# Kernel optimization log

Hardware: AMD Instinct MI355X
Metric: run time of the kernel (lower is better)

Reference implementation:

```python
import jax, jax.numpy as jnp
import numpy as np

BOUNDS = 1.3
RES = 512
N_COMP = 16
N_LAMB = 3        # n_lamb_params[0]
VEC_PARAM = 3     # vecSize_params[0]
OUT_DIM = 32
N_PTS = 2097152

MAT_X = np.array([0, 0, 1])  # matMode first coord per plane
MAT_Y = np.array([1, 2, 2])  # matMode second coord per plane
VEC_M = np.array([2, 1, 0])  # vecMode


def _sample2d(grid, x, y):
    # grid: [C,H,W]; x,y: [N] in [-1,1]; bilinear, align_corners=True
    C, H, W = grid.shape
    ix = (x + 1.0) * 0.5 * (W - 1)
    iy = (y + 1.0) * 0.5 * (H - 1)
    x0 = jnp.floor(ix)
    y0 = jnp.floor(iy)
    wx = ix - x0
    wy = iy - y0
    x0i = jnp.clip(x0.astype(jnp.int32), 0, W - 1)
    x1i = jnp.clip(x0i + 1, 0, W - 1)
    y0i = jnp.clip(y0.astype(jnp.int32), 0, H - 1)
    y1i = jnp.clip(y0i + 1, 0, H - 1)
    g = lambda yi, xi: grid[:, yi, xi]  # [C,N]
    return (g(y0i, x0i) * (1 - wy) * (1 - wx) + g(y0i, x1i) * (1 - wy) * wx
            + g(y1i, x0i) * wy * (1 - wx) + g(y1i, x1i) * wy * wx)


def _sample1d(vec, y):
    # vec: [C,L]; y: [N] in [-1,1]; linear interp along L (grid width is 1,
    # x coord is always 0 in the torch code so it reduces to 1D)
    C, L = vec.shape
    iy = (y + 1.0) * 0.5 * (L - 1)
    y0 = jnp.floor(iy)
    wy = iy - y0
    y0i = jnp.clip(y0.astype(jnp.int32), 0, L - 1)
    y1i = jnpp_clip = jnp.clip(y0i + 1, 0, L - 1)
    return vec[:, y0i] * (1 - wy) + vec[:, y1i] * wy


def setup_inputs() -> dict:
    key = jax.random.key(0)
    k1, k2, k3, k4, k5 = jax.random.split(key, 5)
    pts = (jax.random.uniform(k1, (N_PTS, 3), jnp.float32) * 2.0 - 1.0) * BOUNDS
    timestamps = jax.random.uniform(k2, (N_PTS, 1), jnp.float32) * 2.0 - 1.0
    scale = 0.1
    planes = scale * jax.random.normal(k3, (3, N_COMP, RES, RES), jnp.float32)
    lines = scale * jax.random.normal(k4, (3, N_COMP, RES), jnp.float32)
    params_grid = scale * jnp.ones((N_LAMB, VEC_PARAM), jnp.float32)
    # torch Linear(19 -> 32, bias=False): weight [out, in]
    W = jax.random.normal(k5, (OUT_DIM, N_COMP + N_LAMB), jnp.float32) * (1.0 / np.sqrt(N_COMP + N_LAMB))
    return {"pts": pts, "timestamps": timestamps, "planes": planes,
            "lines": lines, "params_grid": params_grid, "W": W}


def reference(pts, timestamps, planes, lines, params_grid, W):
    # normalize_aabb with aabb = [[b,b,b],[-b,-b,-b]]
    pts_n = (pts - BOUNDS) * (2.0 / (-2.0 * BOUNDS)) - 1.0  # -> [-1,1]
    # torch code detaches sampling coordinates
    pts_n = jax.lax.stop_gradient(pts_n)
    t = jax.lax.stop_gradient(timestamps[:, 0])
    plane_x = pts_n[:, MAT_X].T  # [3,N]
    plane_y = pts_n[:, MAT_Y].T  # [3,N]
    line_c = pts_n[:, VEC_M].T   # [3,N]
    plane_feat = jax.vmap(_sample2d)(planes, plane_x, plane_y)  # [3,C,N]
    line_feat = jax.vmap(_sample1d)(lines, line_c)              # [3,C,N]
    coef = jnp.sum(plane_feat * line_feat, axis=0)              # [C,N]
    pfeat = _sample1d(params_grid, t)                           # [3,N]
    feats = jnp.concatenate([coef, pfeat], axis=0).T            # [N,19]
    return feats @ W.T                                          # [N,32]
```

## Files before the change

### kernel.cpp

```cpp
#include <hip/hip_runtime.h>
#include <hip/hip_bf16.h>

#define RES 512
#define NC 16
#define NPLANES 3
#define NB 32
#define NCELLS (NB * NB * NB)

typedef float f32x4 __attribute__((ext_vector_type(4)));

static __device__ inline float nt_loadf(const float* p) { return __builtin_nontemporal_load(p); }
static __device__ inline void nt_store4(float* p, f32x4 v) {
  __builtin_nontemporal_store(v, (f32x4*)p);
}
static __device__ inline float bf_lo(unsigned u) { return __uint_as_float(u << 16); }
static __device__ inline float bf_hi(unsigned u) { return __uint_as_float(u & 0xFFFF0000u); }

#define NORM_K ((float)(2.0 / (-2.0 * 1.3)))

__global__ __launch_bounds__(256) void transpose_planes_k(
    const float* __restrict__ in, __hip_bfloat16* __restrict__ out)
{
  __shared__ float sm[NC][64 + 1];
  int b   = blockIdx.x;
  int xb  = b & 7;
  int y   = (b >> 3) & 511;
  int p   = b >> 12;
  int x0  = xb << 6;
  int tid = threadIdx.x;
#pragma unroll
  for (int k = 0; k < 4; ++k) {
    int e = tid + k * 256;
    int c = e >> 6, x = e & 63;
    sm[c][x] = nt_loadf(&in[(size_t)((p * NC + c) * RES + y) * RES + x0 + x]);
  }
  __syncthreads();
#pragma unroll
  for (int k = 0; k < 4; ++k) {
    int e = tid + k * 256;
    int x = e >> 4, c = e & 15;
    out[(size_t)((p * RES + y) * RES + x0 + x) * NC + c] = __float2bfloat16(sm[c][x]);
  }
}

__global__ void transpose_lines_k(const float* __restrict__ in, float* __restrict__ out)
{
  int i = blockIdx.x * 256 + threadIdx.x;
  if (i >= NPLANES * RES * NC) return;
  int c = i & 15;
  int l = (i >> 4) & 511;
  int p = i >> 13;
  out[i] = nt_loadf(&in[(p * NC + c) * RES + l]);
}

static __device__ inline int cell_of(float px, float py, float pz)
{
  float n0 = (px - 1.3f) * NORM_K - 1.0f;
  float n1 = (py - 1.3f) * NORM_K - 1.0f;
  float n2 = (pz - 1.3f) * NORM_K - 1.0f;
  int cx = (int)((n0 + 1.0f) * 16.0f); cx = cx < 0 ? 0 : (cx > NB - 1 ? NB - 1 : cx);
  int cy = (int)((n1 + 1.0f) * 16.0f); cy = cy < 0 ? 0 : (cy > NB - 1 ? NB - 1 : cy);
  int cz = (int)((n2 + 1.0f) * 16.0f); cz = cz < 0 ? 0 : (cz > NB - 1 ? NB - 1 : cz);
  return (cx << 10) | (cy << 5) | cz;
}

__global__ void zero_hist_k(unsigned* __restrict__ hist)
{
  int i = blockIdx.x * 256 + threadIdx.x;
  if (i < NCELLS) hist[i] = 0;
}

__global__ __launch_bounds__(256) void histrank_k(
    const float* __restrict__ pts, unsigned* __restrict__ hist,
    unsigned* __restrict__ key, unsigned* __restrict__ rank, int N)
{
  int base = (blockIdx.x * 256 + threadIdx.x) * 4;
  if (base >= N) return;
  uint4 kv, rv;
  if (base + 4 <= N) {
    const f32x4* p4 = (const f32x4*)(pts + 3 * (size_t)base);
    f32x4 a = p4[0], b = p4[1], c = p4[2];
    int c0 = cell_of(a.x, a.y, a.z);
    int c1 = cell_of(a.w, b.x, b.y);
    int c2 = cell_of(b.z, b.w, c.x);
    int c3 = cell_of(c.y, c.z, c.w);
    kv.x = c0; kv.y = c1; kv.z = c2; kv.w = c3;
    rv.x = atomicAdd(&hist[c0], 1u);
    rv.y = atomicAdd(&hist[c1], 1u);
    rv.z = atomicAdd(&hist[c2], 1u);
    rv.w = atomicAdd(&hist[c3], 1u);
    *(uint4*)(key + base)  = kv;
    *(uint4*)(rank + base) = rv;
  } else {
    for (int j = 0; j < 4 && base + j < N; ++j) {
      int i = base + j;
      int cc = cell_of(pts[3 * i], pts[3 * i + 1], pts[3 * i + 2]);
      key[i]  = cc;
      rank[i] = atomicAdd(&hist[cc], 1u);
    }
  }
}

__global__ __launch_bounds__(256) void prefix_k(
    const unsigned* __restrict__ hist, unsigned* __restrict__ offs)
{
  __shared__ unsigned s[256];
  int t = threadIdx.x;
  unsigned sum = 0;
  for (int k = 0; k < NCELLS / 256; ++k) sum += hist[t * (NCELLS / 256) + k];
  s[t] = sum;
  __syncthreads();
  for (int d = 1; d < 256; d <<= 1) {
    unsigned v = (t >= d) ? s[t - d] : 0u;
    __syncthreads();
    s[t] += v;
    __syncthreads();
  }
  unsigned run = (t == 0) ? 0u : s[t - 1];
  for (int k = 0; k < NCELLS / 256; ++k) {
    int c = t * (NCELLS / 256) + k;
    offs[c] = run;
    run += hist[c];
  }
}

__global__ __launch_bounds__(256) void scatter_k(
    const float* __restrict__ pts, const float* __restrict__ ts,
    const unsigned* __restrict__ key, const unsigned* __restrict__ rank,
    const unsigned* __restrict__ offs, f32x4* __restrict__ rec,
    unsigned* __restrict__ oidx, int N)
{
  int base = (blockIdx.x * 256 + threadIdx.x) * 4;
  if (base >= N) return;
  if (base + 4 <= N) {
    uint4 kv = *(const uint4*)(key + base);
    uint4 rv = *(const uint4*)(rank + base);
    const f32x4* p4 = (const f32x4*)(pts + 3 * (size_t)base);
    f32x4 a = p4[0], b = p4[1], c = p4[2];
    f32x4 tv = *(const f32x4*)(ts + base);
    unsigned p0 = offs[kv.x] + rv.x;
    unsigned p1 = offs[kv.y] + rv.y;
    unsigned p2 = offs[kv.z] + rv.z;
    unsigned p3 = offs[kv.w] + rv.w;
    f32x4 r0; r0.x = a.x; r0.y = a.y; r0.z = a.z; r0.w = tv.x;
    f32x4 r1; r1.x = a.w; r1.y = b.x; r1.z = b.y; r1.w = tv.y;
    f32x4 r2; r2.x = b.z; r2.y = b.w; r2.z = c.x; r2.w = tv.z;
    f32x4 r3; r3.x = c.y; r3.y = c.z; r3.z = c.w; r3.w = tv.w;
    rec[p0] = r0; rec[p1] = r1; rec[p2] = r2; rec[p3] = r3;
    oidx[p0] = base + 0; oidx[p1] = base + 1;
    oidx[p2] = base + 2; oidx[p3] = base + 3;
  } else {
    for (int j = 0; j < 4 && base + j < N; ++j) {
      int i = base + j;
      unsigned pos = offs[key[i]] + rank[i];
      f32x4 r; r.x = pts[3 * i]; r.y = pts[3 * i + 1]; r.z = pts[3 * i + 2];
      r.w = ts[i];
      rec[pos] = r;
      oidx[pos] = i;
    }
  }
}

__global__ __launch_bounds__(256) void visnerf_sorted_k(
    const f32x4* __restrict__ rec, const unsigned* __restrict__ oidx,
    const __hip_bfloat16* __restrict__ planesb, const float* __restrict__ lines,
    const float* __restrict__ pg, const float* __restrict__ W,
    float* __restrict__ out, int N)
{
  __shared__ __align__(16) float sW[32 * 20];
  __shared__ __align__(16) float st[256 * 16];
  __shared__ float spg[9];
  int tid = threadIdx.x;
  for (int e = tid; e < 640; e += 256) {
    int o = e / 20, c = e - o * 20;
    sW[e] = (c < 19) ? W[o * 19 + c] : 0.0f;
  }
  if (tid < 9) spg[tid] = pg[tid];
  __syncthreads();

  int nwg = gridDim.x, bid = blockIdx.x;
  int sbid = ((nwg & 7) == 0) ? ((bid & 7) * (nwg >> 3) + (bid >> 3)) : bid;
  int j  = sbid * 256 + tid;
  int jc = (j < N) ? j : (N - 1);

  f32x4 r = rec[jc];
  unsigned oi = oidx[jc];
  float t = r.w;

  float nn[3];
  nn[0] = (r.x - 1.3f) * NORM_K - 1.0f;
  nn[1] = (r.y - 1.3f) * NORM_K - 1.0f;
  nn[2] = (r.z - 1.3f) * NORM_K - 1.0f;

  float feats[20];
#pragma unroll
  for (int c = 0; c < 20; ++c) feats[c] = 0.0f;

  const int matx[3] = {0, 0, 1};
  const int maty[3] = {1, 2, 2};
  const int vecm[3] = {2, 1, 0};

#pragma unroll
  for (int q = 0; q < 3; ++q) {
    float x  = nn[matx[q]], y = nn[maty[q]], lc = nn[vecm[q]];
    float ix = (x + 1.0f) * 0.5f * (float)(RES - 1);
    float iy = (y + 1.0f) * 0.5f * (float)(RES - 1);
    float fx = floorf(ix), fy = floorf(iy);
    float wx = ix - fx, wy = iy - fy;
    int x0 = (int)fx; x0 = x0 < 0 ? 0 : (x0 > RES - 1 ? RES - 1 : x0);
    int y0 = (int)fy; y0 = y0 < 0 ? 0 : (y0 > RES - 1 ? RES - 1 : y0);
    int x1 = (x0 + 1 > RES - 1) ? RES - 1 : x0 + 1;
    int y1 = (y0 + 1 > RES - 1) ? RES - 1 : y0 + 1;

    float il = (lc + 1.0f) * 0.5f * (float)(RES - 1);
    float fl = floorf(il);
    float wl = il - fl;
    int l0 = (int)fl; l0 = l0 < 0 ? 0 : (l0 > RES - 1 ? RES - 1 : l0);
    int l1 = (l0 + 1 > RES - 1) ? RES - 1 : l0 + 1;

    float w00 = (1.0f - wy) * (1.0f - wx);
    float w01 = (1.0f - wy) * wx;
    float w10 = wy * (1.0f - wx);
    float w11 = wy * wx;
    float wl0 = 1.0f - wl;

    const uint4* ta = (const uint4*)(planesb + (size_t)((q * RES + y0) * RES + x0) * NC);
    const uint4* tb = (const uint4*)(planesb + (size_t)((q * RES + y0) * RES + x1) * NC);
    const uint4* tc = (const uint4*)(planesb + (size_t)((q * RES + y1) * RES + x0) * NC);
    const uint4* td = (const uint4*)(planesb + (size_t)((q * RES + y1) * RES + x1) * NC);
    const float4* L0 = (const float4*)(lines + (size_t)(q * RES + l0) * NC);
    const float4* L1 = (const float4*)(lines + (size_t)(q * RES + l1) * NC);
#pragma unroll
    for (int h = 0; h < 2; ++h) {
      uint4 ua = ta[h], ub = tb[h], uc = tc[h], ud = td[h];
      float4 e0a = L0[2 * h + 0], e0b = L0[2 * h + 1];
      float4 e1a = L1[2 * h + 0], e1b = L1[2 * h + 1];
      const unsigned* pa = &ua.x;
      const unsigned* pb = &ub.x;
      const unsigned* pc = &uc.x;
      const unsigned* pd = &ud.x;
      const float* q0 = &e0a.x;
      const float* q1 = &e1a.x;
#pragma unroll
      for (int w = 0; w < 4; ++w) {
        int c0 = h * 8 + 2 * w;
        float pf0 = w00 * bf_lo(pa[w]) + w01 * bf_lo(pb[w]) +
                    w10 * bf_lo(pc[w]) + w11 * bf_lo(pd[w]);
        float pf1 = w00 * bf_hi(pa[w]) + w01 * bf_hi(pb[w]) +
                    w10 * bf_hi(pc[w]) + w11 * bf_hi(pd[w]);
        float lf0 = (w < 2) ? (wl0 * q0[2 * w] + wl * q1[2 * w])
                            : (wl0 * (&e0b.x)[2 * w - 4] + wl * (&e1b.x)[2 * w - 4]);
        float lf1 = (w < 2) ? (wl0 * q0[2 * w + 1] + wl * q1[2 * w + 1])
                            : (wl0 * (&e0b.x)[2 * w - 3] + wl * (&e1b.x)[2 * w - 3]);
        feats[c0 + 0] += pf0 * lf0;
        feats[c0 + 1] += pf1 * lf1;
      }
    }
  }

  {
    float it = (t + 1.0f) * 0.5f * 2.0f;
    float ft = floorf(it);
    float wt = it - ft;
    int t0 = (int)ft; t0 = t0 < 0 ? 0 : (t0 > 2 ? 2 : t0);
    int t1 = (t0 + 1 > 2) ? 2 : t0 + 1;
    feats[16] = spg[0 + t0] * (1.0f - wt) + spg[0 + t1] * wt;
    feats[17] = spg[3 + t0] * (1.0f - wt) + spg[3 + t1] * wt;
    feats[18] = spg[6 + t0] * (1.0f - wt) + spg[6 + t1] * wt;
    feats[19] = 0.0f;
  }

  int lane  = tid & 63;
  int wbase = tid & ~63;
  int chunk = lane & 3;
  int psel  = lane >> 2;
#pragma unroll
  for (int ph = 0; ph < 2; ++ph) {
#pragma unroll
    for (int o = 0; o < 16; ++o) {
      int oo = ph * 16 + o;
      const float4* wr = (const float4*)(sW + oo * 20);
      float acc = 0.0f;
#pragma unroll
      for (int k = 0; k < 5; ++k) {
        float4 wv = wr[k];
        acc += feats[4 * k + 0] * wv.x + feats[4 * k + 1] * wv.y +
               feats[4 * k + 2] * wv.z + feats[4 * k + 3] * wv.w;
      }
      st[tid * 16 + ((o + (tid >> 1)) & 15)] = acc;
    }
#pragma unroll
    for (int g = 0; g < 4; ++g) {
      int owner_lane = g * 16 + psel;
      int pt = wbase + owner_lane;
      int jp = sbid * 256 + pt;
      unsigned oi_p = (unsigned)__shfl((int)oi, owner_lane, 64);
      f32x4 v;
#pragma unroll
      for (int jj = 0; jj < 4; ++jj) {
        int o = chunk * 4 + jj;
        v[jj] = st[pt * 16 + ((o + (pt >> 1)) & 15)];
      }
      if (jp < N) nt_store4(out + (size_t)oi_p * 32 + ph * 16 + chunk * 4, v);
    }
  }
}

template <bool TP>
__global__ __launch_bounds__(256) void visnerf_main_k(
    const float* __restrict__ pts, const float* __restrict__ ts,
    const __hip_bfloat16* __restrict__ planesb, const float* __restrict__ lines,
    const float* __restrict__ planes_f32, const float* __restrict__ lines_f32,
    const float* __restrict__ pg, const float* __restrict__ W,
    float* __restrict__ out, int N)
{
  __shared__ __align__(16) float sW[32 * 20];
  __shared__ __align__(16) float st[256 * 32];
  __shared__ float spg[9];
  int tid = threadIdx.x;
  for (int e = tid; e < 640; e += 256) {
    int o = e / 20, c = e - o * 20;
    sW[e] = (c < 19) ? W[o * 19 + c] : 0.0f;
  }
  if (tid < 9) spg[tid] = pg[tid];
  __syncthreads();

  int i  = blockIdx.x * 256 + tid;
  int ii = (i < N) ? i : (N - 1);
  float px = nt_loadf(&pts[ii * 3 + 0]);
  float py = nt_loadf(&pts[ii * 3 + 1]);
  float pz = nt_loadf(&pts[ii * 3 + 2]);
  float t  = nt_loadf(&ts[ii]);

  float nn[3];
  nn[0] = (px - 1.3f) * NORM_K - 1.0f;
  nn[1] = (py - 1.3f) * NORM_K - 1.0f;
  nn[2] = (pz - 1.3f) * NORM_K - 1.0f;

  float feats[20];
#pragma unroll
  for (int c = 0; c < 20; ++c) feats[c] = 0.0f;

  const int matx[3] = {0, 0, 1};
  const int maty[3] = {1, 2, 2};
  const int vecm[3] = {2, 1, 0};

#pragma unroll
  for (int q = 0; q < 3; ++q) {
    float x  = nn[matx[q]], y = nn[maty[q]], lc = nn[vecm[q]];
    float ix = (x + 1.0f) * 0.5f * (float)(RES - 1);
    float iy = (y + 1.0f) * 0.5f * (float)(RES - 1);
    float fx = floorf(ix), fy = floorf(iy);
    float wx = ix - fx, wy = iy - fy;
    int x0 = (int)fx; x0 = x0 < 0 ? 0 : (x0 > RES - 1 ? RES - 1 : x0);
    int y0 = (int)fy; y0 = y0 < 0 ? 0 : (y0 > RES - 1 ? RES - 1 : y0);
    int x1 = (x0 + 1 > RES - 1) ? RES - 1 : x0 + 1;
    int y1 = (y0 + 1 > RES - 1) ? RES - 1 : y0 + 1;

    float il = (lc + 1.0f) * 0.5f * (float)(RES - 1);
    float fl = floorf(il);
    float wl = il - fl;
    int l0 = (int)fl; l0 = l0 < 0 ? 0 : (l0 > RES - 1 ? RES - 1 : l0);
    int l1 = (l0 + 1 > RES - 1) ? RES - 1 : l0 + 1;

    float w00 = (1.0f - wy) * (1.0f - wx);
    float w01 = (1.0f - wy) * wx;
    float w10 = wy * (1.0f - wx);
    float w11 = wy * wx;
    float wl0 = 1.0f - wl;

    if (TP) {
      const uint4* ta = (const uint4*)(planesb + (size_t)((q * RES + y0) * RES + x0) * NC);
      const uint4* tb = (const uint4*)(planesb + (size_t)((q * RES + y0) * RES + x1) * NC);
      const uint4* tc = (const uint4*)(planesb + (size_t)((q * RES + y1) * RES + x0) * NC);
      const uint4* td = (const uint4*)(planesb + (size_t)((q * RES + y1) * RES + x1) * NC);
      const float4* L0 = (const float4*)(lines + (size_t)(q * RES + l0) * NC);
      const float4* L1 = (const float4*)(lines + (size_t)(q * RES + l1) * NC);
#pragma unroll
      for (int h = 0; h < 2; ++h) {
        uint4 ua = ta[h], ub = tb[h], uc = tc[h], ud = td[h];
        float4 e0a = L0[2 * h + 0], e0b = L0[2 * h + 1];
        float4 e1a = L1[2 * h + 0], e1b = L1[2 * h + 1];
        const unsigned* pa = &ua.x;
        const unsigned* pb = &ub.x;
        const unsigned* pc = &uc.x;
        const unsigned* pd = &ud.x;
        const float* q0 = &e0a.x;
        const float* q1 = &e1a.x;
#pragma unroll
        for (int w = 0; w < 4; ++w) {
          int c0 = h * 8 + 2 * w;
          float pf0 = w00 * bf_lo(pa[w]) + w01 * bf_lo(pb[w]) +
                      w10 * bf_lo(pc[w]) + w11 * bf_lo(pd[w]);
          float pf1 = w00 * bf_hi(pa[w]) + w01 * bf_hi(pb[w]) +
                      w10 * bf_hi(pc[w]) + w11 * bf_hi(pd[w]);
          float lf0 = (w < 2) ? (wl0 * q0[2 * w] + wl * q1[2 * w])
                              : (wl0 * (&e0b.x)[2 * w - 4] + wl * (&e1b.x)[2 * w - 4]);
          float lf1 = (w < 2) ? (wl0 * q0[2 * w + 1] + wl * q1[2 * w + 1])
                              : (wl0 * (&e0b.x)[2 * w - 3] + wl * (&e1b.x)[2 * w - 3]);
          feats[c0 + 0] += pf0 * lf0;
          feats[c0 + 1] += pf1 * lf1;
        }
      }
    } else {
#pragma unroll 4
      for (int c = 0; c < NC; ++c) {
        const float* pl = planes_f32 + (size_t)(q * NC + c) * RES * RES;
        float a  = pl[y0 * RES + x0], b = pl[y0 * RES + x1];
        float c2 = pl[y1 * RES + x0], d = pl[y1 * RES + x1];
        const float* ln = lines_f32 + (size_t)(q * NC + c) * RES;
        float lf = ln[l0] * wl0 + ln[l1] * wl;
        feats[c] += (w00 * a + w01 * b + w10 * c2 + w11 * d) * lf;
      }
    }
  }

  {
    float it = (t + 1.0f) * 0.5f * 2.0f;
    float ft = floorf(it);
    float wt = it - ft;
    int t0 = (int)ft; t0 = t0 < 0 ? 0 : (t0 > 2 ? 2 : t0);
    int t1 = (t0 + 1 > 2) ? 2 : t0 + 1;
    feats[16] = spg[0 + t0] * (1.0f - wt) + spg[0 + t1] * wt;
    feats[17] = spg[3 + t0] * (1.0f - wt) + spg[3 + t1] * wt;
    feats[18] = spg[6 + t0] * (1.0f - wt) + spg[6 + t1] * wt;
    feats[19] = 0.0f;
  }

  float res[32];
#pragma unroll
  for (int o = 0; o < 32; ++o) {
    const float4* wr = (const float4*)(sW + o * 20);
    float acc = 0.0f;
#pragma unroll
    for (int k = 0; k < 5; ++k) {
      float4 wv = wr[k];
      acc += feats[4 * k + 0] * wv.x + feats[4 * k + 1] * wv.y +
             feats[4 * k + 2] * wv.z + feats[4 * k + 3] * wv.w;
    }
    res[o] = acc;
  }

#pragma unroll
  for (int o = 0; o < 32; ++o)
    st[tid * 32 + ((o + tid) & 31)] = res[o];
  __syncthreads();

  size_t gbase = (size_t)blockIdx.x * 8192;
  size_t total = (size_t)N * 32;
#pragma unroll
  for (int k = 0; k < 8; ++k) {
    int idx = tid + k * 256;
    int j   = idx * 4;
    int pq  = j >> 5;
    f32x4 v;
    v.x = st[pq * 32 + (((j & 31) + 0 + pq) & 31)];
    v.y = st[pq * 32 + (((j & 31) + 1 + pq) & 31)];
    v.z = st[pq * 32 + (((j & 31) + 2 + pq) & 31)];
    v.w = st[pq * 32 + (((j & 31) + 3 + pq) & 31)];
    if (gbase + j + 4 <= total) {
      nt_store4(out + gbase + j, v);
    }
  }
}

extern "C" void kernel_launch(void* const* d_in, const int* in_sizes, int n_in,
                              void* d_out, int out_size, void* d_ws, size_t ws_size,
                              hipStream_t stream)
{
  const float* pts    = (const float*)d_in[0];
  const float* ts     = (const float*)d_in[1];
  const float* planes = (const float*)d_in[2];
  const float* lines  = (const float*)d_in[3];
  const float* pg     = (const float*)d_in[4];
  const float* W      = (const float*)d_in[5];
  float* out = (float*)d_out;
  int N = in_sizes[0] / 3;
  int blocksN = (N + 255) / 256;
  int blocks4 = (N + 1023) / 1024;

  auto align256 = [](size_t x) { return (x + 255) & ~(size_t)255; };
  size_t planesTb_bytes = align256((size_t)NPLANES * RES * RES * NC * 2);
  size_t linesT_bytes   = align256((size_t)NPLANES * RES * NC * 4);
  size_t hist_bytes     = align256((size_t)NCELLS * 4);
  size_t offs_bytes     = align256((size_t)NCELLS * 4);
  size_t key_bytes      = align256((size_t)N * 4);
  size_t rank_bytes     = align256((size_t)N * 4);
  size_t oidx_bytes     = align256((size_t)N * 4);
  size_t rec_bytes      = align256((size_t)N * 16);
  size_t sorted_total = planesTb_bytes + linesT_bytes + hist_bytes + offs_bytes +
                        key_bytes + rank_bytes + oidx_bytes + rec_bytes;

  if (ws_size >= sorted_total) {
    char* p = (char*)d_ws;
    __hip_bfloat16* planesTb = (__hip_bfloat16*)p;       p += planesTb_bytes;
    float*    linesT = (float*)p;                        p += linesT_bytes;
    unsigned* hist   = (unsigned*)p;                     p += hist_bytes;
    unsigned* offs   = (unsigned*)p;                     p += offs_bytes;
    unsigned* key    = (unsigned*)p;                     p += key_bytes;
    unsigned* rank   = (unsigned*)p;                     p += rank_bytes;
    unsigned* oidx   = (unsigned*)p;                     p += oidx_bytes;
    f32x4*    rec    = (f32x4*)p;

    transpose_planes_k<<<NPLANES * RES * (RES / 64), 256, 0, stream>>>(planes, planesTb);
    transpose_lines_k<<<(NPLANES * RES * NC + 255) / 256, 256, 0, stream>>>(lines, linesT);
    zero_hist_k<<<(NCELLS + 255) / 256, 256, 0, stream>>>(hist);
    histrank_k<<<blocks4, 256, 0, stream>>>(pts, hist, key, rank, N);
    prefix_k<<<1, 256, 0, stream>>>(hist, offs);
    scatter_k<<<blocks4, 256, 0, stream>>>(pts, ts, key, rank, offs, rec, oidx, N);
    visnerf_sorted_k<<<blocksN, 256, 0, stream>>>(rec, oidx, planesTb, linesT,
                                                  pg, W, out, N);
  } else if (ws_size >= planesTb_bytes + linesT_bytes) {
    __hip_bfloat16* planesTb = (__hip_bfloat16*)d_ws;
    float* linesT = (float*)((char*)d_ws + planesTb_bytes);
    transpose_planes_k<<<NPLANES * RES * (RES / 64), 256, 0, stream>>>(planes, planesTb);
    transpose_lines_k<<<(NPLANES * RES * NC + 255) / 256, 256, 0, stream>>>(lines, linesT);
    visnerf_main_k<true><<<blocksN, 256, 0, stream>>>(
        pts, ts, planesTb, linesT, nullptr, nullptr, pg, W, out, N);
  } else {
    visnerf_main_k<false><<<blocksN, 256, 0, stream>>>(
        pts, ts, nullptr, nullptr, planes, lines, pg, W, out, N);
  }
}
```

Baseline: 317.7 us.

## Parallelize cell prefix scan across blocks and recompute cell keys in scatter

Replaces the single-block serial-per-thread prefix sum over 32768 cells with a three-kernel block-parallel scan (per-block scan, scan of block sums, add-back). Also drops the per-point key array and instead recomputes the cell index from the points in the scatter kernel, removing an 8 MB write and read. This adds two extra kernel launches and a little recomputation in exchange.

```diff
diff --git a/kernel.cpp b/kernel.cpp
--- a/kernel.cpp
+++ b/kernel.cpp
@@ -72,11 +72,10 @@
 
 __global__ __launch_bounds__(256) void histrank_k(
     const float* __restrict__ pts, unsigned* __restrict__ hist,
-    unsigned* __restrict__ key, unsigned* __restrict__ rank, int N)
+    unsigned* __restrict__ rank, int N)
 {
   int base = (blockIdx.x * 256 + threadIdx.x) * 4;
   if (base >= N) return;
-  uint4 kv, rv;
   if (base + 4 <= N) {
     const f32x4* p4 = (const f32x4*)(pts + 3 * (size_t)base);
     f32x4 a = p4[0], b = p4[1], c = p4[2];
@@ -84,64 +83,83 @@
     int c1 = cell_of(a.w, b.x, b.y);
     int c2 = cell_of(b.z, b.w, c.x);
     int c3 = cell_of(c.y, c.z, c.w);
-    kv.x = c0; kv.y = c1; kv.z = c2; kv.w = c3;
+    uint4 rv;
     rv.x = atomicAdd(&hist[c0], 1u);
     rv.y = atomicAdd(&hist[c1], 1u);
     rv.z = atomicAdd(&hist[c2], 1u);
     rv.w = atomicAdd(&hist[c3], 1u);
-    *(uint4*)(key + base)  = kv;
     *(uint4*)(rank + base) = rv;
   } else {
     for (int j = 0; j < 4 && base + j < N; ++j) {
       int i = base + j;
       int cc = cell_of(pts[3 * i], pts[3 * i + 1], pts[3 * i + 2]);
-      key[i]  = cc;
       rank[i] = atomicAdd(&hist[cc], 1u);
     }
   }
 }
 
-__global__ __launch_bounds__(256) void prefix_k(
-    const unsigned* __restrict__ hist, unsigned* __restrict__ offs)
+__global__ __launch_bounds__(256) void scan1_k(
+    const unsigned* __restrict__ hist, unsigned* __restrict__ offs,
+    unsigned* __restrict__ bsum)
 {
   __shared__ unsigned s[256];
-  int t = threadIdx.x;
-  unsigned sum = 0;
-  for (int k = 0; k < NCELLS / 256; ++k) sum += hist[t * (NCELLS / 256) + k];
-  s[t] = sum;
+  int b = blockIdx.x, t = threadIdx.x;
+  unsigned v = hist[b * 256 + t];
+  s[t] = v;
   __syncthreads();
   for (int d = 1; d < 256; d <<= 1) {
-    unsigned v = (t >= d) ? s[t - d] : 0u;
+    unsigned u = (t >= d) ? s[t - d] : 0u;
     __syncthreads();
-    s[t] += v;
+    s[t] += u;
     __syncthreads();
   }
-  unsigned run = (t == 0) ? 0u : s[t - 1];
-  for (int k = 0; k < NCELLS / 256; ++k) {
-    int c = t * (NCELLS / 256) + k;
-    offs[c] = run;
-    run += hist[c];
-  }
+  offs[b * 256 + t] = s[t] - v;
+  if (t == 255) bsum[b] = s[255];
+}
+
+__global__ __launch_bounds__(128) void scan2_k(unsigned* __restrict__ bsum)
+{
+  __shared__ unsigned s[128];
+  int t = threadIdx.x;
+  unsigned v = bsum[t];
+  s[t] = v;
+  __syncthreads();
+  for (int d = 1; d < 128; d <<= 1) {
+    unsigned u = (t >= d) ? s[t - d] : 0u;
+    __syncthreads();
+    s[t] += u;
+    __syncthreads();
+  }
+  bsum[t] = s[t] - v;
+}
+
+__global__ __launch_bounds__(256) void scan3_k(
+    unsigned* __restrict__ offs, const unsigned* __restrict__ bsum)
+{
+  int i = blockIdx.x * 256 + threadIdx.x;
+  if (i < NCELLS) offs[i] += bsum[i >> 8];
 }
 
 __global__ __launch_bounds__(256) void scatter_k(
     const float* __restrict__ pts, const float* __restrict__ ts,
-    const unsigned* __restrict__ key, const unsigned* __restrict__ rank,
-    const unsigned* __restrict__ offs, f32x4* __restrict__ rec,
-    unsigned* __restrict__ oidx, int N)
+    const unsigned* __restrict__ rank, const unsigned* __restrict__ offs,
+    f32x4* __restrict__ rec, unsigned* __restrict__ oidx, int N)
 {
   int base = (blockIdx.x * 256 + threadIdx.x) * 4;
   if (base >= N) return;
   if (base + 4 <= N) {
-    uint4 kv = *(const uint4*)(key + base);
     uint4 rv = *(const uint4*)(rank + base);
     const f32x4* p4 = (const f32x4*)(pts + 3 * (size_t)base);
     f32x4 a = p4[0], b = p4[1], c = p4[2];
     f32x4 tv = *(const f32x4*)(ts + base);
-    unsigned p0 = offs[kv.x] + rv.x;
-    unsigned p1 = offs[kv.y] + rv.y;
-    unsigned p2 = offs[kv.z] + rv.z;
-    unsigned p3 = offs[kv.w] + rv.w;
+    int c0 = cell_of(a.x, a.y, a.z);
+    int c1 = cell_of(a.w, b.x, b.y);
+    int c2 = cell_of(b.z, b.w, c.x);
+    int c3 = cell_of(c.y, c.z, c.w);
+    unsigned p0 = offs[c0] + rv.x;
+    unsigned p1 = offs[c1] + rv.y;
+    unsigned p2 = offs[c2] + rv.z;
+    unsigned p3 = offs[c3] + rv.w;
     f32x4 r0; r0.x = a.x; r0.y = a.y; r0.z = a.z; r0.w = tv.x;
     f32x4 r1; r1.x = a.w; r1.y = b.x; r1.z = b.y; r1.w = tv.y;
     f32x4 r2; r2.x = b.z; r2.y = b.w; r2.z = c.x; r2.w = tv.z;
@@ -152,7 +170,8 @@
   } else {
     for (int j = 0; j < 4 && base + j < N; ++j) {
       int i = base + j;
-      unsigned pos = offs[key[i]] + rank[i];
+      int cc = cell_of(pts[3 * i], pts[3 * i + 1], pts[3 * i + 2]);
+      unsigned pos = offs[cc] + rank[i];
       f32x4 r; r.x = pts[3 * i]; r.y = pts[3 * i + 1]; r.z = pts[3 * i + 2];
       r.w = ts[i];
       rec[pos] = r;
@@ -484,12 +503,12 @@
   size_t linesT_bytes   = align256((size_t)NPLANES * RES * NC * 4);
   size_t hist_bytes     = align256((size_t)NCELLS * 4);
   size_t offs_bytes     = align256((size_t)NCELLS * 4);
-  size_t key_bytes      = align256((size_t)N * 4);
+  size_t bsum_bytes     = align256((size_t)128 * 4);
   size_t rank_bytes     = align256((size_t)N * 4);
   size_t oidx_bytes     = align256((size_t)N * 4);
   size_t rec_bytes      = align256((size_t)N * 16);
   size_t sorted_total = planesTb_bytes + linesT_bytes + hist_bytes + offs_bytes +
-                        key_bytes + rank_bytes + oidx_bytes + rec_bytes;
+                        bsum_bytes + rank_bytes + oidx_bytes + rec_bytes;
 
   if (ws_size >= sorted_total) {
     char* p = (char*)d_ws;
@@ -497,7 +516,7 @@
     float*    linesT = (float*)p;                        p += linesT_bytes;
     unsigned* hist   = (unsigned*)p;                     p += hist_bytes;
     unsigned* offs   = (unsigned*)p;                     p += offs_bytes;
-    unsigned* key    = (unsigned*)p;                     p += key_bytes;
+    unsigned* bsum   = (unsigned*)p;                     p += bsum_bytes;
     unsigned* rank   = (unsigned*)p;                     p += rank_bytes;
     unsigned* oidx   = (unsigned*)p;                     p += oidx_bytes;
     f32x4*    rec    = (f32x4*)p;
@@ -505,9 +524,11 @@
     transpose_planes_k<<<NPLANES * RES * (RES / 64), 256, 0, stream>>>(planes, planesTb);
     transpose_lines_k<<<(NPLANES * RES * NC + 255) / 256, 256, 0, stream>>>(lines, linesT);
     zero_hist_k<<<(NCELLS + 255) / 256, 256, 0, stream>>>(hist);
-    histrank_k<<<blocks4, 256, 0, stream>>>(pts, hist, key, rank, N);
-    prefix_k<<<1, 256, 0, stream>>>(hist, offs);
-    scatter_k<<<blocks4, 256, 0, stream>>>(pts, ts, key, rank, offs, rec, oidx, N);
+    histrank_k<<<blocks4, 256, 0, stream>>>(pts, hist, rank, N);
+    scan1_k<<<NCELLS / 256, 256, 0, stream>>>(hist, offs, bsum);
+    scan2_k<<<1, 128, 0, stream>>>(bsum);
+    scan3_k<<<NCELLS / 256, 256, 0, stream>>>(offs, bsum);
+    scatter_k<<<blocks4, 256, 0, stream>>>(pts, ts, rank, offs, rec, oidx, N);
     visnerf_sorted_k<<<blocksN, 256, 0, stream>>>(rec, oidx, planesTb, linesT,
                                                   pg, W, out, N);
   } else if (ws_size >= planesTb_bytes + linesT_bytes) {
```

Result: faster. 306.8 us (-3.4%).
